# Performance work log

Hardware: AMD Instinct MI355X
Metric: run time of the kernel (lower is better)

The kernel has to match this reference:

```python
import jax, jax.numpy as jnp
import numpy as np

B, S = 512, 2048
E_DIM, P_DIM, C_DIM, H_DIM = 64, 32, 64, 64
NEG = jnp.float32(-2**32 + 1)  # padding value used by the torch module


def setup_inputs() -> dict:
    key = jax.random.key(0)
    ks = jax.random.split(key, 9)
    return {
        "seq_items": jax.random.normal(ks[0], (B, S, E_DIM), dtype=jnp.float32),
        "seq_pos": jax.random.normal(ks[1], (B, S, P_DIM), dtype=jnp.float32),
        "target_item": jax.random.normal(ks[2], (B, C_DIM), dtype=jnp.float32),
        "Wp": jax.random.normal(ks[3], (P_DIM, H_DIM), dtype=jnp.float32) * (2.0 / (P_DIM + H_DIM)) ** 0.5,
        "We": jax.random.normal(ks[4], (E_DIM, H_DIM), dtype=jnp.float32) * (2.0 / (E_DIM + H_DIM)) ** 0.5,
        "Wc": jax.random.normal(ks[5], (C_DIM, H_DIM), dtype=jnp.float32) * (2.0 / (C_DIM + H_DIM)) ** 0.5,
        "b": jnp.zeros((H_DIM,), dtype=jnp.float32),
        "z": jnp.ones((H_DIM,), dtype=jnp.float32),
        "seq_len": jax.random.randint(ks[6], (B,), 0, S, dtype=jnp.int32),
    }


def reference(seq_items, seq_pos, target_item, Wp, We, Wc, b, z, seq_len):
    # Projections: [B,h] and [B,S,h]
    out_c = target_item @ Wc                      # [B, h]
    out_e = jnp.einsum("bse,eh->bsh", seq_items, We)
    out_p = jnp.einsum("bsp,ph->bsh", seq_pos, Wp)
    # Additive attention score: [B, S]
    a = jnp.sum(jnp.tanh(out_c[:, None, :] + out_p + out_e + b) * z, axis=-1)
    # seq_len mask
    mask = jnp.arange(seq_items.shape[1])[None, :] < seq_len[:, None]  # [B, S]
    score = jax.nn.softmax(jnp.where(mask, a, NEG), axis=1)            # [B, S]
    # u = score @ e -> [B, 1, e_dim]  (intended unsqueeze(1) matmul)
    u = jnp.einsum("bs,bse->be", score, seq_items)[:, None, :]
    # r = sum of masked raw scores -> [B, 1]
    r = jnp.sum(jnp.where(mask, a, 0.0), axis=1, keepdims=True)
    return (u, r)
```

## Files before the change

### kernel.cpp

```cpp
#include <hip/hip_runtime.h>
#include <math.h>

#define B_ 512
#define S_ 2048
#define E_DIM 64
#define P_DIM 32
#define H_DIM 64
#define CB_STRIDE 68

typedef short s16x8 __attribute__((ext_vector_type(8)));
typedef float f32x4 __attribute__((ext_vector_type(4)));

__device__ __forceinline__ float wave_reduce_sum(float v) {
#pragma unroll
  for (int m = 32; m >= 1; m >>= 1) v += __shfl_xor(v, m, 64);
  return v;
}

__device__ __forceinline__ float wave_reduce_max(float v) {
#pragma unroll
  for (int m = 32; m >= 1; m >>= 1) v = fmaxf(v, __shfl_xor(v, m, 64));
  return v;
}

__device__ __forceinline__ float tanh_fast(float x) {
  float e = __expf(2.0f * x);
  return 1.0f - 2.0f * __builtin_amdgcn_rcpf(e + 1.0f);
}

__device__ __forceinline__ short bf16b(float x) {
  union { float f; unsigned u; } a;
  a.f = x;
  unsigned r = (a.u + 0x7FFFu + ((a.u >> 16) & 1u)) >> 16;
  return (short)r;
}

__global__ __launch_bounds__(256) void scores_mfma_kernel(
    const float* __restrict__ seq_items, const float* __restrict__ seq_pos,
    const float* __restrict__ target_item, const float* __restrict__ Wp,
    const float* __restrict__ We, const float* __restrict__ Wc,
    const float* __restrict__ bias, const float* __restrict__ z,
    const int* __restrict__ seq_len, float* __restrict__ chunk_buf) {
  const int blk = blockIdx.x;
  const int b = blk >> 4;
  const int s0 = (blk & 15) << 7;
  const int L = seq_len[b];
  const bool uni = (L == 0);
  if (!uni && s0 >= L) return;

  __shared__ s16x8 lds_b[12 * 64];
  __shared__ float c_part[4 * 64];
  __shared__ float s_a[128];
  __shared__ float s_w[128];
  __shared__ __align__(16) float s_pc[4 * 64];
  __shared__ float redm[4], reds[4], redr[4];

  const int tid = threadIdx.x;
  const int l = tid & 63;
  const int w = tid >> 6;
  const int cc = l & 15;
  const int q = l >> 4;

#pragma unroll
  for (int i = 0; i < 3; ++i) {
    const int f = w * 3 + i;
    const int kstep = f >> 2;
    const int nt = f & 3;
    const float* __restrict__ src =
        (kstep < 2) ? (We + (size_t)(kstep * 32 + q * 8) * H_DIM + nt * 16 + cc)
                    : (Wp + (size_t)(q * 8) * H_DIM + nt * 16 + cc);
    s16x8 v;
#pragma unroll
    for (int j = 0; j < 8; ++j) v[j] = bf16b(src[(size_t)j * H_DIM]);
    lds_b[f * 64 + l] = v;
  }

  {
    const float* __restrict__ tg = target_item + b * 64;
    float cp = (w == 0) ? bias[l] : 0.0f;
#pragma unroll
    for (int e = 0; e < 16; ++e)
      cp = fmaf(tg[w * 16 + e], Wc[(w * 16 + e) * H_DIM + l], cp);
    c_part[w * 64 + l] = cp;
  }
  __syncthreads();

  s16x8 bfr[12];
#pragma unroll
  for (int f = 0; f < 12; ++f) bfr[f] = lds_b[f * 64 + l];

  float ch[4], zh[4];
#pragma unroll
  for (int nt = 0; nt < 4; ++nt) {
    const int h = nt * 16 + cc;
    ch[nt] = c_part[h] + c_part[64 + h] + c_part[128 + h] + c_part[192 + h];
    zh[nt] = z[h];
  }

  const float* __restrict__ itemsB = seq_items + (size_t)b * S_ * E_DIM;
  const float* __restrict__ posB = seq_pos + (size_t)b * S_ * P_DIM;

#pragma unroll
  for (int mt = 0; mt < 2; ++mt) {
    const int rb = s0 + w * 32 + mt * 16;
    const int s = rb + cc;
    f32x4 acc[4] = {};

#pragma unroll
    for (int kk = 0; kk < 2; ++kk) {
      const float* __restrict__ p = itemsB + (size_t)s * E_DIM + kk * 32 + q * 8;
      const float4 x0 = ((const float4*)p)[0];
      const float4 x1 = ((const float4*)p)[1];
      s16x8 af;
      af[0] = bf16b(x0.x); af[1] = bf16b(x0.y);
      af[2] = bf16b(x0.z); af[3] = bf16b(x0.w);
      af[4] = bf16b(x1.x); af[5] = bf16b(x1.y);
      af[6] = bf16b(x1.z); af[7] = bf16b(x1.w);
#pragma unroll
      for (int nt = 0; nt < 4; ++nt)
        acc[nt] = __builtin_amdgcn_mfma_f32_16x16x32_bf16(af, bfr[kk * 4 + nt],
                                                          acc[nt], 0, 0, 0);
    }
    {
      const float* __restrict__ p = posB + (size_t)s * P_DIM + q * 8;
      const float4 x0 = ((const float4*)p)[0];
      const float4 x1 = ((const float4*)p)[1];
      s16x8 af;
      af[0] = bf16b(x0.x); af[1] = bf16b(x0.y);
      af[2] = bf16b(x0.z); af[3] = bf16b(x0.w);
      af[4] = bf16b(x1.x); af[5] = bf16b(x1.y);
      af[6] = bf16b(x1.z); af[7] = bf16b(x1.w);
#pragma unroll
      for (int nt = 0; nt < 4; ++nt)
        acc[nt] = __builtin_amdgcn_mfma_f32_16x16x32_bf16(af, bfr[8 + nt],
                                                          acc[nt], 0, 0, 0);
    }

    float asum[4];
#pragma unroll
    for (int r = 0; r < 4; ++r) {
      float t = tanh_fast(acc[0][r] + ch[0]) * zh[0];
      t += tanh_fast(acc[1][r] + ch[1]) * zh[1];
      t += tanh_fast(acc[2][r] + ch[2]) * zh[2];
      t += tanh_fast(acc[3][r] + ch[3]) * zh[3];
      asum[r] = t;
    }
#pragma unroll
    for (int r = 0; r < 4; ++r) {
#pragma unroll
      for (int m = 8; m >= 1; m >>= 1) asum[r] += __shfl_xor(asum[r], m, 64);
    }
    if (cc == 0) {
#pragma unroll
      for (int r = 0; r < 4; ++r) s_a[w * 32 + mt * 16 + q * 4 + r] = asum[r];
    }
  }

  __syncthreads();
  const int row = tid & 127;
  const int srow = s0 + row;
  const bool valid = uni || (srow < L);
  const float araw = s_a[row];
  const float ae = uni ? 0.0f : araw;
  float mp = wave_reduce_max(valid ? ae : -INFINITY);
  if (l == 0) redm[w] = mp;
  __syncthreads();
  const float mc = fmaxf(fmaxf(redm[0], redm[1]), fmaxf(redm[2], redm[3]));
  const float wgt = valid ? __expf(ae - mc) : 0.0f;
  if (tid < 128) s_w[row] = wgt;
  const float scp = wave_reduce_sum(wgt);
  const float rap = wave_reduce_sum(valid ? ae : 0.0f);
  if (l == 0) { reds[w] = scp; redr[w] = rap; }
  __syncthreads();

  {
    const int e4 = l & 15;
    const int rr = l >> 4;
    const float4* __restrict__ ip4 =
        (const float4*)(itemsB + (size_t)(s0 + w * 32) * E_DIM);
    float4 a4 = make_float4(0.f, 0.f, 0.f, 0.f);
#pragma unroll
    for (int i = 0; i < 8; ++i) {
      const int rloc = rr + i * 4;
      const float g = s_w[w * 32 + rloc];
      const float4 x = ip4[rloc * 16 + e4];
      a4.x = fmaf(g, x.x, a4.x);
      a4.y = fmaf(g, x.y, a4.y);
      a4.z = fmaf(g, x.z, a4.z);
      a4.w = fmaf(g, x.w, a4.w);
    }
#pragma unroll
    for (int m = 16; m <= 32; m <<= 1) {
      a4.x += __shfl_xor(a4.x, m, 64);
      a4.y += __shfl_xor(a4.y, m, 64);
      a4.z += __shfl_xor(a4.z, m, 64);
      a4.w += __shfl_xor(a4.w, m, 64);
    }
    if (rr == 0) *(float4*)&s_pc[w * 64 + e4 * 4] = a4;
  }
  __syncthreads();

  float* __restrict__ cb = chunk_buf + (size_t)blk * CB_STRIDE;
  if (tid < 64) {
    cb[tid] = s_pc[tid] + s_pc[64 + tid] + s_pc[128 + tid] + s_pc[192 + tid];
  } else if (tid == 64) {
    cb[64] = mc;
  } else if (tid == 65) {
    cb[65] = reds[0] + reds[1];
  } else if (tid == 66) {
    cb[66] = redr[0] + redr[1];
  }
}

__global__ __launch_bounds__(64) void combine_kernel(
    const float* __restrict__ chunk_buf, const int* __restrict__ seq_len,
    float* __restrict__ out) {
  const int b = blockIdx.x;
  const int t = threadIdx.x;
  const int L = seq_len[b];
  const int nc = (L == 0) ? 16 : ((L + 127) >> 7);
  const float* __restrict__ cb = chunk_buf + (size_t)b * 16 * CB_STRIDE;

  float m = -INFINITY;
  for (int c = 0; c < nc; ++c) m = fmaxf(m, cb[c * CB_STRIDE + 64]);
  float u = 0.0f, den = 0.0f, r = 0.0f;
  for (int c = 0; c < nc; ++c) {
    const float e = __expf(cb[c * CB_STRIDE + 64] - m);
    u = fmaf(e, cb[c * CB_STRIDE + t], u);
    den = fmaf(e, cb[c * CB_STRIDE + 65], den);
    r += cb[c * CB_STRIDE + 66];
  }
  out[b * E_DIM + t] = u / den;
  if (t == 0) out[B_ * E_DIM + b] = r;
}

extern "C" void kernel_launch(void* const* d_in, const int* in_sizes, int n_in,
                              void* d_out, int out_size, void* d_ws, size_t ws_size,
                              hipStream_t stream) {
  const float* seq_items = (const float*)d_in[0];
  const float* seq_pos = (const float*)d_in[1];
  const float* target_item = (const float*)d_in[2];
  const float* Wp = (const float*)d_in[3];
  const float* We = (const float*)d_in[4];
  const float* Wc = (const float*)d_in[5];
  const float* Wc_ = Wc;
  const float* bias = (const float*)d_in[6];
  const float* z = (const float*)d_in[7];
  const int* seq_len = (const int*)d_in[8];
  float* out = (float*)d_out;
  float* chunk_buf = (float*)d_ws;

  scores_mfma_kernel<<<B_ * 16, 256, 0, stream>>>(
      seq_items, seq_pos, target_item, Wp, We, Wc_, bias, z, seq_len, chunk_buf);
  combine_kernel<<<B_, 64, 0, stream>>>(chunk_buf, seq_len, out);
}
```

Baseline: 458.7 us.

## Hoist weight fragments and context projection into a precompute kernel; batch input loads

Adds a small precompute kernel that converts the We/Wp weights into bf16 MFMA fragments once and computes the target projection plus bias for every batch. The main kernel then reads these from global memory instead of rebuilding them per block, which removes a barrier and redundant per-block work. It also issues all the item and position loads up front before any MFMA, and uses packed bf16 conversion intrinsics. The cost is an extra kernel launch and additional workspace traffic.

```diff
diff --git a/kernel.cpp b/kernel.cpp
--- a/kernel.cpp
+++ b/kernel.cpp
@@ -1,4 +1,5 @@
 #include <hip/hip_runtime.h>
+#include <hip/hip_bf16.h>
 #include <math.h>
 
 #define B_ 512
@@ -9,6 +10,7 @@
 #define CB_STRIDE 68
 
 typedef short s16x8 __attribute__((ext_vector_type(8)));
+typedef int i32x4 __attribute__((ext_vector_type(4)));
 typedef float f32x4 __attribute__((ext_vector_type(4)));
 
 __device__ __forceinline__ float wave_reduce_sum(float v) {
@@ -35,12 +37,62 @@
   return (short)r;
 }
 
+__device__ __forceinline__ int cvt_pk2(float a, float b) {
+  union { __hip_bfloat162 v; int i; } u;
+  u.v = __float22bfloat162_rn(make_float2(a, b));
+  return u.i;
+}
+
+__device__ __forceinline__ s16x8 cvt8(float4 lo, float4 hi) {
+  i32x4 r;
+  r[0] = cvt_pk2(lo.x, lo.y);
+  r[1] = cvt_pk2(lo.z, lo.w);
+  r[2] = cvt_pk2(hi.x, hi.y);
+  r[3] = cvt_pk2(hi.z, hi.w);
+  return __builtin_bit_cast(s16x8, r);
+}
+
+__global__ __launch_bounds__(256) void precompute_kernel(
+    const float* __restrict__ target_item, const float* __restrict__ Wp,
+    const float* __restrict__ We, const float* __restrict__ Wc,
+    const float* __restrict__ bias, s16x8* __restrict__ frags,
+    float* __restrict__ c_all) {
+  const int tid = threadIdx.x;
+  const int l = tid & 63;
+  if (blockIdx.x == 0) {
+    const int w = tid >> 6;
+    const int cc = l & 15;
+    const int q = l >> 4;
+#pragma unroll
+    for (int i = 0; i < 3; ++i) {
+      const int f = w * 3 + i;
+      const int kstep = f >> 2;
+      const int nt = f & 3;
+      const float* __restrict__ src =
+          (kstep < 2)
+              ? (We + (size_t)(kstep * 32 + q * 8) * H_DIM + nt * 16 + cc)
+              : (Wp + (size_t)(q * 8) * H_DIM + nt * 16 + cc);
+      s16x8 v;
+#pragma unroll
+      for (int j = 0; j < 8; ++j) v[j] = bf16b(src[(size_t)j * H_DIM]);
+      frags[f * 64 + l] = v;
+    }
+  } else {
+    const int b = (blockIdx.x - 1) * 4 + (tid >> 6);
+    const int h = l;
+    const float* __restrict__ tg = target_item + b * E_DIM;
+    float c = bias[h];
+#pragma unroll
+    for (int e = 0; e < 64; ++e) c = fmaf(tg[e], Wc[e * H_DIM + h], c);
+    c_all[b * H_DIM + h] = c;
+  }
+}
+
 __global__ __launch_bounds__(256) void scores_mfma_kernel(
     const float* __restrict__ seq_items, const float* __restrict__ seq_pos,
-    const float* __restrict__ target_item, const float* __restrict__ Wp,
-    const float* __restrict__ We, const float* __restrict__ Wc,
-    const float* __restrict__ bias, const float* __restrict__ z,
-    const int* __restrict__ seq_len, float* __restrict__ chunk_buf) {
+    const float* __restrict__ z, const int* __restrict__ seq_len,
+    const s16x8* __restrict__ frags, const float* __restrict__ c_all,
+    float* __restrict__ chunk_buf) {
   const int blk = blockIdx.x;
   const int b = blk >> 4;
   const int s0 = (blk & 15) << 7;
@@ -48,8 +100,6 @@
   const bool uni = (L == 0);
   if (!uni && s0 >= L) return;
 
-  __shared__ s16x8 lds_b[12 * 64];
-  __shared__ float c_part[4 * 64];
   __shared__ float s_a[128];
   __shared__ float s_w[128];
   __shared__ __align__(16) float s_pc[4 * 64];
@@ -61,80 +111,58 @@
   const int cc = l & 15;
   const int q = l >> 4;
 
-#pragma unroll
-  for (int i = 0; i < 3; ++i) {
-    const int f = w * 3 + i;
-    const int kstep = f >> 2;
-    const int nt = f & 3;
-    const float* __restrict__ src =
-        (kstep < 2) ? (We + (size_t)(kstep * 32 + q * 8) * H_DIM + nt * 16 + cc)
-                    : (Wp + (size_t)(q * 8) * H_DIM + nt * 16 + cc);
-    s16x8 v;
-#pragma unroll
-    for (int j = 0; j < 8; ++j) v[j] = bf16b(src[(size_t)j * H_DIM]);
-    lds_b[f * 64 + l] = v;
-  }
-
-  {
-    const float* __restrict__ tg = target_item + b * 64;
-    float cp = (w == 0) ? bias[l] : 0.0f;
-#pragma unroll
-    for (int e = 0; e < 16; ++e)
-      cp = fmaf(tg[w * 16 + e], Wc[(w * 16 + e) * H_DIM + l], cp);
-    c_part[w * 64 + l] = cp;
-  }
-  __syncthreads();
-
   s16x8 bfr[12];
 #pragma unroll
-  for (int f = 0; f < 12; ++f) bfr[f] = lds_b[f * 64 + l];
+  for (int f = 0; f < 12; ++f) bfr[f] = frags[f * 64 + l];
 
   float ch[4], zh[4];
 #pragma unroll
   for (int nt = 0; nt < 4; ++nt) {
     const int h = nt * 16 + cc;
-    ch[nt] = c_part[h] + c_part[64 + h] + c_part[128 + h] + c_part[192 + h];
+    ch[nt] = c_all[b * H_DIM + h];
     zh[nt] = z[h];
   }
 
   const float* __restrict__ itemsB = seq_items + (size_t)b * S_ * E_DIM;
   const float* __restrict__ posB = seq_pos + (size_t)b * S_ * P_DIM;
 
+  float4 xi[2][4];
+  float4 xp[2][2];
 #pragma unroll
   for (int mt = 0; mt < 2; ++mt) {
-    const int rb = s0 + w * 32 + mt * 16;
-    const int s = rb + cc;
+    const int s = s0 + w * 32 + mt * 16 + cc;
+    const float* __restrict__ pi = itemsB + (size_t)s * E_DIM + q * 8;
+    xi[mt][0] = ((const float4*)pi)[0];
+    xi[mt][1] = ((const float4*)pi)[1];
+    xi[mt][2] = ((const float4*)(pi + 32))[0];
+    xi[mt][3] = ((const float4*)(pi + 32))[1];
+    const float* __restrict__ pp = posB + (size_t)s * P_DIM + q * 8;
+    xp[mt][0] = ((const float4*)pp)[0];
+    xp[mt][1] = ((const float4*)pp)[1];
+  }
+
+  s16x8 afr[2][3];
+#pragma unroll
+  for (int mt = 0; mt < 2; ++mt) {
+    afr[mt][0] = cvt8(xi[mt][0], xi[mt][1]);
+    afr[mt][1] = cvt8(xi[mt][2], xi[mt][3]);
+    afr[mt][2] = cvt8(xp[mt][0], xp[mt][1]);
+  }
+
+#pragma unroll
+  for (int mt = 0; mt < 2; ++mt) {
     f32x4 acc[4] = {};
-
 #pragma unroll
     for (int kk = 0; kk < 2; ++kk) {
-      const float* __restrict__ p = itemsB + (size_t)s * E_DIM + kk * 32 + q * 8;
-      const float4 x0 = ((const float4*)p)[0];
-      const float4 x1 = ((const float4*)p)[1];
-      s16x8 af;
-      af[0] = bf16b(x0.x); af[1] = bf16b(x0.y);
-      af[2] = bf16b(x0.z); af[3] = bf16b(x0.w);
-      af[4] = bf16b(x1.x); af[5] = bf16b(x1.y);
-      af[6] = bf16b(x1.z); af[7] = bf16b(x1.w);
 #pragma unroll
       for (int nt = 0; nt < 4; ++nt)
-        acc[nt] = __builtin_amdgcn_mfma_f32_16x16x32_bf16(af, bfr[kk * 4 + nt],
-                                                          acc[nt], 0, 0, 0);
-    }
-    {
-      const float* __restrict__ p = posB + (size_t)s * P_DIM + q * 8;
-      const float4 x0 = ((const float4*)p)[0];
-      const float4 x1 = ((const float4*)p)[1];
-      s16x8 af;
-      af[0] = bf16b(x0.x); af[1] = bf16b(x0.y);
-      af[2] = bf16b(x0.z); af[3] = bf16b(x0.w);
-      af[4] = bf16b(x1.x); af[5] = bf16b(x1.y);
-      af[6] = bf16b(x1.z); af[7] = bf16b(x1.w);
-#pragma unroll
-      for (int nt = 0; nt < 4; ++nt)
-        acc[nt] = __builtin_amdgcn_mfma_f32_16x16x32_bf16(af, bfr[8 + nt],
-                                                          acc[nt], 0, 0, 0);
-    }
+        acc[nt] = __builtin_amdgcn_mfma_f32_16x16x32_bf16(
+            afr[mt][kk], bfr[kk * 4 + nt], acc[nt], 0, 0, 0);
+    }
+#pragma unroll
+    for (int nt = 0; nt < 4; ++nt)
+      acc[nt] = __builtin_amdgcn_mfma_f32_16x16x32_bf16(
+          afr[mt][2], bfr[8 + nt], acc[nt], 0, 0, 0);
 
     float asum[4];
 #pragma unroll
@@ -243,14 +271,20 @@
   const float* Wp = (const float*)d_in[3];
   const float* We = (const float*)d_in[4];
   const float* Wc = (const float*)d_in[5];
-  const float* Wc_ = Wc;
   const float* bias = (const float*)d_in[6];
   const float* z = (const float*)d_in[7];
   const int* seq_len = (const int*)d_in[8];
   float* out = (float*)d_out;
+
   float* chunk_buf = (float*)d_ws;
-
-  scores_mfma_kernel<<<B_ * 16, 256, 0, stream>>>(
-      seq_items, seq_pos, target_item, Wp, We, Wc_, bias, z, seq_len, chunk_buf);
+  float* c_all = (float*)d_ws + (size_t)B_ * 16 * CB_STRIDE;
+  s16x8* frags =
+      (s16x8*)((float*)d_ws + (size_t)B_ * 16 * CB_STRIDE + B_ * H_DIM);
+
+  precompute_kernel<<<129, 256, 0, stream>>>(target_item, Wp, We, Wc, bias,
+                                             frags, c_all);
+  scores_mfma_kernel<<<B_ * 16, 256, 0, stream>>>(seq_items, seq_pos, z,
+                                                  seq_len, frags, c_all,
+                                                  chunk_buf);
   combine_kernel<<<B_, 64, 0, stream>>>(chunk_buf, seq_len, out);
 }
```

New measurement: 439.6 us, median of 2. 1.04x faster.
